# Kernel tuning notes

Measured on AMD Instinct MI355X. Metric: run time of the kernel, lower is better.

The kernel has to match this reference:

```python
import jax, jax.numpy as jnp
import numpy as np

N_NODES = 50000
N_EDGES = 800000
DIM = 128


def setup_inputs() -> dict:
    key = jax.random.key(0)
    ks = jax.random.split(key, 8)
    scale = 1.0 / np.sqrt(DIM)
    z = jax.random.normal(ks[0], (N_NODES, DIM), dtype=jnp.float32)
    Wq = jax.random.normal(ks[1], (DIM, DIM), dtype=jnp.float32) * scale
    Wk = jax.random.normal(ks[2], (DIM, DIM), dtype=jnp.float32) * scale
    Wv = jax.random.normal(ks[3], (DIM, DIM), dtype=jnp.float32) * scale
    bq = jnp.zeros((DIM,), dtype=jnp.float32)
    bk = jnp.zeros((DIM,), dtype=jnp.float32)
    bv = jnp.zeros((DIM,), dtype=jnp.float32)
    src = jax.random.randint(ks[4], (N_EDGES,), 0, N_NODES, dtype=jnp.int32)
    dst = jax.random.randint(ks[5], (N_EDGES,), 0, N_NODES, dtype=jnp.int32)
    return {"z": z, "Wq": Wq, "bq": bq, "Wk": Wk, "bk": bk,
            "Wv": Wv, "bv": bv, "src": src, "dst": dst}


def reference(z, Wq, bq, Wk, bk, Wv, bv, src, dst):
    tau = 1.0 / np.sqrt(z.shape[-1] * 1.0)  # 1/sqrt(out_dim), out_dim == DIM
    n = z.shape[0]
    # node-level projections (cheaper than per-edge projection, same math)
    q = z @ Wq + bq          # [N, D]
    k = z @ Wk + bk          # [N, D]
    v = z @ Wv + bv          # [N, D]
    # per-edge unnormalized attention logit: (k_src . q_dst) * tau
    e = jnp.einsum('ed,ed->e', k[src], q[dst]) * jnp.asarray(tau, z.dtype)  # [E]
    # segment softmax over incoming edges of each dst node
    m = jax.ops.segment_max(e, dst, num_segments=n)          # [N], -inf for isolated nodes
    m = jnp.where(jnp.isfinite(m), m, jnp.zeros_like(m))
    ex = jnp.exp(e - m[dst])                                  # [E]
    denom = jax.ops.segment_sum(ex, dst, num_segments=n)      # [N]
    # weighted value aggregation per destination node
    num = jax.ops.segment_sum(ex[:, None] * v[src], dst, num_segments=n)  # [N, D]
    h = num / jnp.where(denom > 0, denom, jnp.ones_like(denom))[:, None]
    return h
```

## Files before the change

kernel.cpp:

```cpp
#include <hip/hip_runtime.h>
#include <math.h>

#define NDIM 128
#define CAP 64

typedef _Float16 half2v __attribute__((ext_vector_type(2)));
typedef _Float16 half4v __attribute__((ext_vector_type(4)));
typedef _Float16 half8v __attribute__((ext_vector_type(8)));
typedef __attribute__((ext_vector_type(4))) float f32x4;

__device__ inline float fdot2h(half2v a, half2v b, float c) {
#if __has_builtin(__builtin_amdgcn_fdot2)
  return __builtin_amdgcn_fdot2(a, b, c, false);
#else
  return fmaf((float)a.x, (float)b.x, fmaf((float)a.y, (float)b.y, c));
#endif
}

__device__ inline half2v h2cast(unsigned u) { return __builtin_bit_cast(half2v, u); }

__global__ __launch_bounds__(256) void prep_kernel(
    const float* __restrict__ Wq, const float* __restrict__ Wk,
    const float* __restrict__ Wv, _Float16* __restrict__ wtf,
    int* __restrict__ cursor, int n) {
  int tid = blockIdx.x * 256 + threadIdx.x;
  if (tid < 3 * NDIM * NDIM) {
    int mat = tid >> 14;
    int rem = tid & 16383;
    int mtg = rem >> 11;
    int kk = (rem >> 9) & 3;
    int lane = (rem >> 3) & 63;
    int j = rem & 7;
    int m = mtg * 16 + (lane & 15);
    int kx = kk * 32 + (lane >> 4) * 8 + j;
    const float* W = (mat == 0) ? Wq : (mat == 1) ? Wk : Wv;
    wtf[tid] = (_Float16)W[kx * NDIM + m];
  }
  int nthr = gridDim.x * 256;
  for (int i = tid; i < n; i += nthr) cursor[i] = 0;
}

__global__ __launch_bounds__(512) void fused_kernel(
    const float* __restrict__ z, const _Float16* __restrict__ wtf,
    const float* __restrict__ bq, const float* __restrict__ bk,
    const float* __restrict__ bv,
    _Float16* __restrict__ qh, _Float16* __restrict__ kh, _Float16* __restrict__ vh,
    int n,
    const int* __restrict__ src, const int* __restrict__ dst,
    int* __restrict__ cursor, int* __restrict__ slots, int ne, int nscat) {
  if ((int)blockIdx.x < nscat) {
    int e = (blockIdx.x * 512 + threadIdx.x) * 4;
    if (e + 3 < ne) {
      int4 d = *(const int4*)(dst + e);
      int4 s = *(const int4*)(src + e);
      int p0 = atomicAdd(&cursor[d.x], 1);
      int p1 = atomicAdd(&cursor[d.y], 1);
      int p2 = atomicAdd(&cursor[d.z], 1);
      int p3 = atomicAdd(&cursor[d.w], 1);
      if (p0 < CAP) slots[(d.x << 6) + p0] = s.x;
      if (p1 < CAP) slots[(d.y << 6) + p1] = s.y;
      if (p2 < CAP) slots[(d.z << 6) + p2] = s.z;
      if (p3 < CAP) slots[(d.w << 6) + p3] = s.w;
    } else {
      for (; e < ne; ++e) {
        int d = dst[e];
        int pos = atomicAdd(&cursor[d], 1);
        if (pos < CAP) slots[(d << 6) + pos] = src[e];
      }
    }
    return;
  }
  int bid = blockIdx.x - nscat;
  int lane = threadIdx.x & 63;
  int w = threadIdx.x >> 6;
  int rowgrp = w >> 1, colhalf = w & 1;
  int l15 = lane & 15, kgrp = lane >> 4;
  int row_b = bid * 64 + rowgrp * 16 + l15;
  bool ok = row_b < n;
  const float* zrow = z + (size_t)row_b * NDIM;
  half8v bfr[4];
#pragma unroll
  for (int kk = 0; kk < 4; ++kk) {
    half8v bv8 = (half8v)0;
    if (ok) {
      const float4* zp = (const float4*)(zrow + kk * 32 + kgrp * 8);
      float4 a0 = zp[0], a1 = zp[1];
      bv8[0] = (_Float16)a0.x; bv8[1] = (_Float16)a0.y;
      bv8[2] = (_Float16)a0.z; bv8[3] = (_Float16)a0.w;
      bv8[4] = (_Float16)a1.x; bv8[5] = (_Float16)a1.y;
      bv8[6] = (_Float16)a1.z; bv8[7] = (_Float16)a1.w;
    }
    bfr[kk] = bv8;
  }
#pragma unroll
  for (int mat = 0; mat < 3; ++mat) {
    const _Float16* wf = wtf + (size_t)mat * NDIM * NDIM;
    const float* bias = (mat == 0) ? bq : (mat == 1) ? bk : bv;
    _Float16* outp = (mat == 0) ? qh : (mat == 1) ? kh : vh;
    f32x4 acc[4];
#pragma unroll
    for (int mt = 0; mt < 4; ++mt) acc[mt] = (f32x4)0.f;
#pragma unroll
    for (int mt = 0; mt < 4; ++mt) {
      int mtg = colhalf * 4 + mt;
#pragma unroll
      for (int kk = 0; kk < 4; ++kk) {
        half8v afr = *(const half8v*)(wf + (((mtg * 4 + kk) * 64) + lane) * 8);
        acc[mt] = __builtin_amdgcn_mfma_f32_16x16x32_f16(afr, bfr[kk], acc[mt],
                                                         0, 0, 0);
      }
    }
    if (ok) {
#pragma unroll
      for (int mt = 0; mt < 4; ++mt) {
        int c0 = colhalf * 64 + mt * 16 + kgrp * 4;
        float4 bb = *(const float4*)(bias + c0);
        half4v pk;
        pk[0] = (_Float16)(acc[mt][0] + bb.x);
        pk[1] = (_Float16)(acc[mt][1] + bb.y);
        pk[2] = (_Float16)(acc[mt][2] + bb.z);
        pk[3] = (_Float16)(acc[mt][3] + bb.w);
        *(half4v*)(outp + (size_t)row_b * NDIM + c0) = pk;
      }
    }
  }
}

__global__ __launch_bounds__(256) void agg_kernel(
    const _Float16* __restrict__ qh, const _Float16* __restrict__ kh,
    const _Float16* __restrict__ vh,
    const int* __restrict__ cursor, const int* __restrict__ slots,
    float* __restrict__ out, int n) {
  int lane = threadIdx.x & 63;
  int node = blockIdx.x * 4 + (threadIdx.x >> 6);
  if (node >= n) return;
  const float tau = 0.08838834764831845f;
  const float M0 = 8.0f;
  int gl = lane & 15;
  int grp = lane >> 4;
  int cnt = cursor[node];
  if (cnt > CAP) cnt = CAP;
  int beg = node << 6;
  uint4 qv = *(const uint4*)(qh + (size_t)node * NDIM + gl * 8);
  half2v q0 = h2cast(qv.x), q1 = h2cast(qv.y), q2 = h2cast(qv.z), q3 = h2cast(qv.w);
  float se = 0.f;
  float h[8];
#pragma unroll
  for (int i = 0; i < 8; ++i) h[i] = 0.f;
  int sj = (lane < cnt) ? slots[beg + lane] : 0;
  int nsub = (cnt + 3) >> 2;
  for (int s = 0; s < nsub; ++s) {
    int j = (s << 2) | grp;
    int row = __shfl(sj, j);
    bool en = j < cnt;
    uint4 kv, vv;
    if (en) {
      kv = *(const uint4*)(kh + (size_t)row * NDIM + gl * 8);
      vv = *(const uint4*)(vh + (size_t)row * NDIM + gl * 8);
    }
    if (en) {
      float p = fdot2h(h2cast(kv.x), q0, 0.f);
      p = fdot2h(h2cast(kv.y), q1, p);
      p = fdot2h(h2cast(kv.z), q2, p);
      p = fdot2h(h2cast(kv.w), q3, p);
      p += __shfl_xor(p, 1);
      p += __shfl_xor(p, 2);
      p += __shfl_xor(p, 4);
      p += __shfl_xor(p, 8);
      float ex = __expf(fmaf(p, tau, -M0));
      se += ex;
      half2v v0 = h2cast(vv.x), v1 = h2cast(vv.y);
      half2v v2 = h2cast(vv.z), v3 = h2cast(vv.w);
      h[0] = fmaf(ex, (float)v0.x, h[0]);
      h[1] = fmaf(ex, (float)v0.y, h[1]);
      h[2] = fmaf(ex, (float)v1.x, h[2]);
      h[3] = fmaf(ex, (float)v1.y, h[3]);
      h[4] = fmaf(ex, (float)v2.x, h[4]);
      h[5] = fmaf(ex, (float)v2.y, h[5]);
      h[6] = fmaf(ex, (float)v3.x, h[6]);
      h[7] = fmaf(ex, (float)v3.y, h[7]);
    }
  }
  se += __shfl_xor(se, 16);
  se += __shfl_xor(se, 32);
#pragma unroll
  for (int i = 0; i < 8; ++i) {
    h[i] += __shfl_xor(h[i], 16);
    h[i] += __shfl_xor(h[i], 32);
  }
  if (grp == 0) {
    float inv = 1.f / ((se > 0.f) ? se : 1.f);
    float4* op = (float4*)(out + (size_t)node * NDIM + gl * 8);
    op[0] = make_float4(h[0] * inv, h[1] * inv, h[2] * inv, h[3] * inv);
    op[1] = make_float4(h[4] * inv, h[5] * inv, h[6] * inv, h[7] * inv);
  }
}

extern "C" void kernel_launch(void* const* d_in, const int* in_sizes, int n_in,
                              void* d_out, int out_size, void* d_ws, size_t ws_size,
                              hipStream_t stream) {
  const float* z  = (const float*)d_in[0];
  const float* Wq = (const float*)d_in[1];
  const float* bq = (const float*)d_in[2];
  const float* Wk = (const float*)d_in[3];
  const float* bk = (const float*)d_in[4];
  const float* Wv = (const float*)d_in[5];
  const float* bv = (const float*)d_in[6];
  const int* src  = (const int*)d_in[7];
  const int* dst  = (const int*)d_in[8];
  int n  = in_sizes[0] / NDIM;
  int ne = in_sizes[7];
  float* out = (float*)d_out;

  char* ws = (char*)d_ws;
  size_t szh = (size_t)n * NDIM * sizeof(_Float16);
  size_t nb = (((size_t)n * sizeof(int)) + 255) & ~(size_t)255;
  size_t off = 0;
  _Float16* qh = (_Float16*)(ws + off); off += szh;
  _Float16* kh = (_Float16*)(ws + off); off += szh;
  _Float16* vh = (_Float16*)(ws + off); off += szh;
  _Float16* wtf = (_Float16*)(ws + off);
  off += ((size_t)3 * NDIM * NDIM * sizeof(_Float16) + 255) & ~(size_t)255;
  int* cursor = (int*)(ws + off); off += nb;
  int* slots  = (int*)(ws + off);

  int nscat = (ne / 4 + 511) / 512;
  int nqkv  = (n + 63) / 64;

  prep_kernel<<<256, 256, 0, stream>>>(Wq, Wk, Wv, wtf, cursor, n);
  fused_kernel<<<nscat + nqkv, 512, 0, stream>>>(z, wtf, bq, bk, bv, qh, kh, vh, n,
                                                 src, dst, cursor, slots, ne, nscat);
  agg_kernel<<<(n + 3) / 4, 256, 0, stream>>>(qh, kh, vh, cursor, slots, out, n);
}
```

Measured before the change: 130.6 us.

## Pad per-node atomic counters to 64 bytes and process two edges per group in aggregation

Each node's edge cursor now sits on its own 64-byte stride (16 ints), so concurrent atomics on neighbouring nodes no longer contend for the same cache line. The aggregation loop now handles two edges per 16-lane group per iteration, with both K/V gathers issued before use, to raise memory-level parallelism and interleave the shuffle reductions. In exchange the cursor array is 16x larger, which means more zeroing work in prep and a larger footprint, and the aggregation kernel uses more registers.

New measurement: 133.3 us. +2.0%, slower.

```diff
diff --git a/kernel.cpp b/kernel.cpp
--- a/kernel.cpp
+++ b/kernel.cpp
@@ -3,6 +3,7 @@
 
 #define NDIM 128
 #define CAP 64
+#define CSTR 16
 
 typedef _Float16 half2v __attribute__((ext_vector_type(2)));
 typedef _Float16 half4v __attribute__((ext_vector_type(4)));
@@ -37,7 +38,8 @@
     wtf[tid] = (_Float16)W[kx * NDIM + m];
   }
   int nthr = gridDim.x * 256;
-  for (int i = tid; i < n; i += nthr) cursor[i] = 0;
+  int tot = n * CSTR;
+  for (int i = tid; i < tot; i += nthr) cursor[i] = 0;
 }
 
 __global__ __launch_bounds__(512) void fused_kernel(
@@ -53,10 +55,10 @@
     if (e + 3 < ne) {
       int4 d = *(const int4*)(dst + e);
       int4 s = *(const int4*)(src + e);
-      int p0 = atomicAdd(&cursor[d.x], 1);
-      int p1 = atomicAdd(&cursor[d.y], 1);
-      int p2 = atomicAdd(&cursor[d.z], 1);
-      int p3 = atomicAdd(&cursor[d.w], 1);
+      int p0 = atomicAdd(&cursor[d.x << 4], 1);
+      int p1 = atomicAdd(&cursor[d.y << 4], 1);
+      int p2 = atomicAdd(&cursor[d.z << 4], 1);
+      int p3 = atomicAdd(&cursor[d.w << 4], 1);
       if (p0 < CAP) slots[(d.x << 6) + p0] = s.x;
       if (p1 < CAP) slots[(d.y << 6) + p1] = s.y;
       if (p2 < CAP) slots[(d.z << 6) + p2] = s.z;
@@ -64,7 +66,7 @@
     } else {
       for (; e < ne; ++e) {
         int d = dst[e];
-        int pos = atomicAdd(&cursor[d], 1);
+        int pos = atomicAdd(&cursor[d << 4], 1);
         if (pos < CAP) slots[(d << 6) + pos] = src[e];
       }
     }
@@ -138,7 +140,7 @@
   const float M0 = 8.0f;
   int gl = lane & 15;
   int grp = lane >> 4;
-  int cnt = cursor[node];
+  int cnt = cursor[node << 4];
   if (cnt > CAP) cnt = CAP;
   int beg = node << 6;
   uint4 qv = *(const uint4*)(qh + (size_t)node * NDIM + gl * 8);
@@ -148,37 +150,69 @@
 #pragma unroll
   for (int i = 0; i < 8; ++i) h[i] = 0.f;
   int sj = (lane < cnt) ? slots[beg + lane] : 0;
-  int nsub = (cnt + 3) >> 2;
+  int nsub = (cnt + 7) >> 3;
   for (int s = 0; s < nsub; ++s) {
-    int j = (s << 2) | grp;
-    int row = __shfl(sj, j);
-    bool en = j < cnt;
-    uint4 kv, vv;
-    if (en) {
-      kv = *(const uint4*)(kh + (size_t)row * NDIM + gl * 8);
-      vv = *(const uint4*)(vh + (size_t)row * NDIM + gl * 8);
-    }
-    if (en) {
-      float p = fdot2h(h2cast(kv.x), q0, 0.f);
-      p = fdot2h(h2cast(kv.y), q1, p);
-      p = fdot2h(h2cast(kv.z), q2, p);
-      p = fdot2h(h2cast(kv.w), q3, p);
-      p += __shfl_xor(p, 1);
-      p += __shfl_xor(p, 2);
-      p += __shfl_xor(p, 4);
-      p += __shfl_xor(p, 8);
-      float ex = __expf(fmaf(p, tau, -M0));
-      se += ex;
-      half2v v0 = h2cast(vv.x), v1 = h2cast(vv.y);
-      half2v v2 = h2cast(vv.z), v3 = h2cast(vv.w);
-      h[0] = fmaf(ex, (float)v0.x, h[0]);
-      h[1] = fmaf(ex, (float)v0.y, h[1]);
-      h[2] = fmaf(ex, (float)v1.x, h[2]);
-      h[3] = fmaf(ex, (float)v1.y, h[3]);
-      h[4] = fmaf(ex, (float)v2.x, h[4]);
-      h[5] = fmaf(ex, (float)v2.y, h[5]);
-      h[6] = fmaf(ex, (float)v3.x, h[6]);
-      h[7] = fmaf(ex, (float)v3.y, h[7]);
+    int j0 = (s << 3) | (grp << 1);
+    int j1 = j0 | 1;
+    int row0 = __shfl(sj, j0);
+    int row1 = __shfl(sj, j1);
+    bool e0 = j0 < cnt, e1 = j1 < cnt;
+    uint4 k0v, v0v, k1v, v1v;
+    if (e0) {
+      k0v = *(const uint4*)(kh + (size_t)row0 * NDIM + gl * 8);
+      v0v = *(const uint4*)(vh + (size_t)row0 * NDIM + gl * 8);
+    }
+    if (e1) {
+      k1v = *(const uint4*)(kh + (size_t)row1 * NDIM + gl * 8);
+      v1v = *(const uint4*)(vh + (size_t)row1 * NDIM + gl * 8);
+    }
+    float pA = 0.f, pB = 0.f;
+    if (e0) {
+      pA = fdot2h(h2cast(k0v.x), q0, 0.f);
+      pA = fdot2h(h2cast(k0v.y), q1, pA);
+      pA = fdot2h(h2cast(k0v.z), q2, pA);
+      pA = fdot2h(h2cast(k0v.w), q3, pA);
+    }
+    if (e1) {
+      pB = fdot2h(h2cast(k1v.x), q0, 0.f);
+      pB = fdot2h(h2cast(k1v.y), q1, pB);
+      pB = fdot2h(h2cast(k1v.z), q2, pB);
+      pB = fdot2h(h2cast(k1v.w), q3, pB);
+    }
+    pA += __shfl_xor(pA, 1);
+    pB += __shfl_xor(pB, 1);
+    pA += __shfl_xor(pA, 2);
+    pB += __shfl_xor(pB, 2);
+    pA += __shfl_xor(pA, 4);
+    pB += __shfl_xor(pB, 4);
+    pA += __shfl_xor(pA, 8);
+    pB += __shfl_xor(pB, 8);
+    float ex0 = e0 ? __expf(fmaf(pA, tau, -M0)) : 0.f;
+    float ex1 = e1 ? __expf(fmaf(pB, tau, -M0)) : 0.f;
+    se += ex0 + ex1;
+    if (e0) {
+      half2v v0 = h2cast(v0v.x), v1 = h2cast(v0v.y);
+      half2v v2 = h2cast(v0v.z), v3 = h2cast(v0v.w);
+      h[0] = fmaf(ex0, (float)v0.x, h[0]);
+      h[1] = fmaf(ex0, (float)v0.y, h[1]);
+      h[2] = fmaf(ex0, (float)v1.x, h[2]);
+      h[3] = fmaf(ex0, (float)v1.y, h[3]);
+      h[4] = fmaf(ex0, (float)v2.x, h[4]);
+      h[5] = fmaf(ex0, (float)v2.y, h[5]);
+      h[6] = fmaf(ex0, (float)v3.x, h[6]);
+      h[7] = fmaf(ex0, (float)v3.y, h[7]);
+    }
+    if (e1) {
+      half2v v0 = h2cast(v1v.x), v1 = h2cast(v1v.y);
+      half2v v2 = h2cast(v1v.z), v3 = h2cast(v1v.w);
+      h[0] = fmaf(ex1, (float)v0.x, h[0]);
+      h[1] = fmaf(ex1, (float)v0.y, h[1]);
+      h[2] = fmaf(ex1, (float)v1.x, h[2]);
+      h[3] = fmaf(ex1, (float)v1.y, h[3]);
+      h[4] = fmaf(ex1, (float)v2.x, h[4]);
+      h[5] = fmaf(ex1, (float)v2.y, h[5]);
+      h[6] = fmaf(ex1, (float)v3.x, h[6]);
+      h[7] = fmaf(ex1, (float)v3.y, h[7]);
     }
   }
   se += __shfl_xor(se, 16);
@@ -214,14 +248,14 @@
 
   char* ws = (char*)d_ws;
   size_t szh = (size_t)n * NDIM * sizeof(_Float16);
-  size_t nb = (((size_t)n * sizeof(int)) + 255) & ~(size_t)255;
   size_t off = 0;
   _Float16* qh = (_Float16*)(ws + off); off += szh;
   _Float16* kh = (_Float16*)(ws + off); off += szh;
   _Float16* vh = (_Float16*)(ws + off); off += szh;
   _Float16* wtf = (_Float16*)(ws + off);
   off += ((size_t)3 * NDIM * NDIM * sizeof(_Float16) + 255) & ~(size_t)255;
-  int* cursor = (int*)(ws + off); off += nb;
+  int* cursor = (int*)(ws + off);
+  off += (((size_t)n * CSTR * sizeof(int)) + 255) & ~(size_t)255;
   int* slots  = (int*)(ws + off);
 
   int nscat = (ne / 4 + 511) / 512;
```

## Replace global per-node atomic scatter with two-phase bucketed partitioning

Applied to the files above, without the earlier changes.

Edge scatter now first buckets edges by dst>>8 into per-bucket partitions, using shared-memory histograms and one global atomic per bucket per block. A new phase-B kernel then places each bucket's edges into per-node slots with shared-memory atomics and writes the node counts. This removes the 800K random global atomics on per-node cursors. In exchange it adds an extra kernel launch and an extra pass through the (src,dst) pairs in a partition buffer. The shared arrays assume nbuck ≤ 256, and each bucket holds at most BCAP entries.

Result: faster. 119.5 us (-8.5%).

```diff
diff --git a/kernel.cpp b/kernel.cpp
--- a/kernel.cpp
+++ b/kernel.cpp
@@ -3,6 +3,7 @@
 
 #define NDIM 128
 #define CAP 64
+#define BCAP 8192
 
 typedef _Float16 half2v __attribute__((ext_vector_type(2)));
 typedef _Float16 half4v __attribute__((ext_vector_type(4)));
@@ -22,7 +23,7 @@
 __global__ __launch_bounds__(256) void prep_kernel(
     const float* __restrict__ Wq, const float* __restrict__ Wk,
     const float* __restrict__ Wv, _Float16* __restrict__ wtf,
-    int* __restrict__ cursor, int n) {
+    int* __restrict__ gcur, int nbuck) {
   int tid = blockIdx.x * 256 + threadIdx.x;
   if (tid < 3 * NDIM * NDIM) {
     int mat = tid >> 14;
@@ -37,7 +38,8 @@
     wtf[tid] = (_Float16)W[kx * NDIM + m];
   }
   int nthr = gridDim.x * 256;
-  for (int i = tid; i < n; i += nthr) cursor[i] = 0;
+  int tot = nbuck * 16;
+  for (int i = tid; i < tot; i += nthr) gcur[i] = 0;
 }
 
 __global__ __launch_bounds__(512) void fused_kernel(
@@ -47,27 +49,48 @@
     _Float16* __restrict__ qh, _Float16* __restrict__ kh, _Float16* __restrict__ vh,
     int n,
     const int* __restrict__ src, const int* __restrict__ dst,
-    int* __restrict__ cursor, int* __restrict__ slots, int ne, int nscat) {
+    int* __restrict__ gcur, int2* __restrict__ part, int ne, int nbuck, int nscat) {
+  __shared__ int lhist[256];
+  __shared__ int lbase[256];
+  __shared__ int lcur[256];
   if ((int)blockIdx.x < nscat) {
-    int e = (blockIdx.x * 512 + threadIdx.x) * 4;
-    if (e + 3 < ne) {
-      int4 d = *(const int4*)(dst + e);
-      int4 s = *(const int4*)(src + e);
-      int p0 = atomicAdd(&cursor[d.x], 1);
-      int p1 = atomicAdd(&cursor[d.y], 1);
-      int p2 = atomicAdd(&cursor[d.z], 1);
-      int p3 = atomicAdd(&cursor[d.w], 1);
-      if (p0 < CAP) slots[(d.x << 6) + p0] = s.x;
-      if (p1 < CAP) slots[(d.y << 6) + p1] = s.y;
-      if (p2 < CAP) slots[(d.z << 6) + p2] = s.z;
-      if (p3 < CAP) slots[(d.w << 6) + p3] = s.w;
+    int tid = threadIdx.x;
+    for (int i = tid; i < nbuck; i += 512) lhist[i] = 0;
+    __syncthreads();
+    int e0 = (blockIdx.x * 512 + tid) * 4;
+    int dd0 = 0, dd1 = 0, dd2 = 0, dd3 = 0, ss0 = 0, ss1 = 0, ss2 = 0, ss3 = 0;
+    bool v0 = false, v1 = false, v2 = false, v3 = false;
+    if (e0 + 3 < ne) {
+      int4 d = *(const int4*)(dst + e0);
+      int4 s = *(const int4*)(src + e0);
+      dd0 = d.x; dd1 = d.y; dd2 = d.z; dd3 = d.w;
+      ss0 = s.x; ss1 = s.y; ss2 = s.z; ss3 = s.w;
+      v0 = v1 = v2 = v3 = true;
     } else {
-      for (; e < ne; ++e) {
-        int d = dst[e];
-        int pos = atomicAdd(&cursor[d], 1);
-        if (pos < CAP) slots[(d << 6) + pos] = src[e];
-      }
-    }
+      if (e0 + 0 < ne) { dd0 = dst[e0 + 0]; ss0 = src[e0 + 0]; v0 = true; }
+      if (e0 + 1 < ne) { dd1 = dst[e0 + 1]; ss1 = src[e0 + 1]; v1 = true; }
+      if (e0 + 2 < ne) { dd2 = dst[e0 + 2]; ss2 = src[e0 + 2]; v2 = true; }
+      if (e0 + 3 < ne) { dd3 = dst[e0 + 3]; ss3 = src[e0 + 3]; v3 = true; }
+    }
+    if (v0) atomicAdd(&lhist[dd0 >> 8], 1);
+    if (v1) atomicAdd(&lhist[dd1 >> 8], 1);
+    if (v2) atomicAdd(&lhist[dd2 >> 8], 1);
+    if (v3) atomicAdd(&lhist[dd3 >> 8], 1);
+    __syncthreads();
+    if (tid < nbuck) {
+      int c = lhist[tid];
+      lbase[tid] = (c > 0) ? atomicAdd(&gcur[tid * 16], c) : 0;
+      lcur[tid] = 0;
+    }
+    __syncthreads();
+    if (v0) { int b = dd0 >> 8; int p = lbase[b] + atomicAdd(&lcur[b], 1);
+              if (p < BCAP) part[b * BCAP + p] = make_int2(ss0, dd0); }
+    if (v1) { int b = dd1 >> 8; int p = lbase[b] + atomicAdd(&lcur[b], 1);
+              if (p < BCAP) part[b * BCAP + p] = make_int2(ss1, dd1); }
+    if (v2) { int b = dd2 >> 8; int p = lbase[b] + atomicAdd(&lcur[b], 1);
+              if (p < BCAP) part[b * BCAP + p] = make_int2(ss2, dd2); }
+    if (v3) { int b = dd3 >> 8; int p = lbase[b] + atomicAdd(&lcur[b], 1);
+              if (p < BCAP) part[b * BCAP + p] = make_int2(ss3, dd3); }
     return;
   }
   int bid = blockIdx.x - nscat;
@@ -124,6 +147,27 @@
       }
     }
   }
+}
+
+__global__ __launch_bounds__(256) void phaseB_kernel(
+    const int2* __restrict__ part, const int* __restrict__ gcur,
+    int* __restrict__ slots, int* __restrict__ cursor, int n) {
+  __shared__ int lcur[256];
+  int tid = threadIdx.x;
+  int nb = blockIdx.x;
+  lcur[tid] = 0;
+  __syncthreads();
+  int cnt = gcur[nb * 16];
+  if (cnt > BCAP) cnt = BCAP;
+  const int2* pp = part + (size_t)nb * BCAP;
+  for (int i = tid; i < cnt; i += 256) {
+    int2 p = pp[i];
+    int r = atomicAdd(&lcur[p.y & 255], 1);
+    if (r < CAP) slots[((size_t)p.y << 6) + r] = p.x;
+  }
+  __syncthreads();
+  int node = nb * 256 + tid;
+  if (node < n) cursor[node] = lcur[tid];
 }
 
 __global__ __launch_bounds__(256) void agg_kernel(
@@ -212,23 +256,31 @@
   int ne = in_sizes[7];
   float* out = (float*)d_out;
 
+  int nbuck = (n + 255) >> 8;
+
   char* ws = (char*)d_ws;
   size_t szh = (size_t)n * NDIM * sizeof(_Float16);
-  size_t nb = (((size_t)n * sizeof(int)) + 255) & ~(size_t)255;
   size_t off = 0;
   _Float16* qh = (_Float16*)(ws + off); off += szh;
   _Float16* kh = (_Float16*)(ws + off); off += szh;
   _Float16* vh = (_Float16*)(ws + off); off += szh;
   _Float16* wtf = (_Float16*)(ws + off);
   off += ((size_t)3 * NDIM * NDIM * sizeof(_Float16) + 255) & ~(size_t)255;
-  int* cursor = (int*)(ws + off); off += nb;
+  int* gcur = (int*)(ws + off);
+  off += (((size_t)nbuck * 16 * sizeof(int)) + 255) & ~(size_t)255;
+  int2* part = (int2*)(ws + off);
+  off += (size_t)nbuck * BCAP * sizeof(int2);
+  int* cursor = (int*)(ws + off);
+  off += (((size_t)n * sizeof(int)) + 255) & ~(size_t)255;
   int* slots  = (int*)(ws + off);
 
   int nscat = (ne / 4 + 511) / 512;
   int nqkv  = (n + 63) / 64;
 
-  prep_kernel<<<256, 256, 0, stream>>>(Wq, Wk, Wv, wtf, cursor, n);
+  prep_kernel<<<256, 256, 0, stream>>>(Wq, Wk, Wv, wtf, gcur, nbuck);
   fused_kernel<<<nscat + nqkv, 512, 0, stream>>>(z, wtf, bq, bk, bv, qh, kh, vh, n,
-                                                 src, dst, cursor, slots, ne, nscat);
+                                                 src, dst, gcur, part, ne, nbuck,
+                                                 nscat);
+  phaseB_kernel<<<nbuck, 256, 0, stream>>>(part, gcur, slots, cursor, n);
   agg_kernel<<<(n + 3) / 4, 256, 0, stream>>>(qh, kh, vh, cursor, slots, out, n);
 }
```
